# Optimization experiments

Hardware: AMD Instinct MI355X
Metric: run time of the kernel (lower is better)

Reference implementation:

```python
import jax, jax.numpy as jnp
import numpy as np

# ---- static config (matches init_kwargs) ----
B, L, D, H, NC = 2, 4096, 256, 8, 3
TOP_N, R = 8, 32              # top_n, vicinity_radius
LS, LE = 1000, 3000           # label_start, label_end
NL = 2                        # n_cross_attn_layers
FF = 4 * D                    # ffn_expand * d_model
Q_MAX = 2 * TOP_N * (2 * R + 1)  # 1040
HD = D // H


def setup_inputs() -> dict:
    key = jax.random.key(0)
    ks = jax.random.split(key, 12)
    def rn(k, shape, s=0.05):
        return jax.random.normal(k, shape, jnp.float32) * s
    return {
        "encoder_output": jax.random.normal(ks[0], (B, L, D), jnp.float32),
        "coarse_logits": jax.random.normal(ks[1], (B, L, NC), jnp.float32),
        "ln_q_g": jnp.ones((NL, D), jnp.float32),
        "ln_q_b": jnp.zeros((NL, D), jnp.float32),
        "ln_kv_g": jnp.ones((NL, D), jnp.float32),
        "ln_kv_b": jnp.zeros((NL, D), jnp.float32),
        "Wq": rn(ks[2], (NL, D, D)), "bq": jnp.zeros((NL, D), jnp.float32),
        "Wk": rn(ks[3], (NL, D, D)), "bk": jnp.zeros((NL, D), jnp.float32),
        "Wv": rn(ks[4], (NL, D, D)), "bv": jnp.zeros((NL, D), jnp.float32),
        "Wo": rn(ks[5], (NL, D, D)), "bo": jnp.zeros((NL, D), jnp.float32),
        "ffn_g": jnp.ones((NL, D), jnp.float32),
        "ffn_b": jnp.zeros((NL, D), jnp.float32),
        "W1": rn(ks[6], (NL, D, FF)), "b1": jnp.zeros((NL, FF), jnp.float32),
        "W2": rn(ks[7], (NL, FF, D)), "b2": jnp.zeros((NL, D), jnp.float32),
        "head_W": rn(ks[8], (D, NC)), "head_b": jnp.zeros((NC,), jnp.float32),
    }


def _layer_norm(x, g, b, eps=1e-5):
    m = jnp.mean(x, axis=-1, keepdims=True)
    v = jnp.mean(jnp.square(x - m), axis=-1, keepdims=True)
    return (x - m) * jax.lax.rsqrt(v + eps) * g + b


def _select_vicinities(coarse_logits):
    # eval mode: no gumbel noise. Returns (vicinity_idx (B,Q_MAX) int32 with
    # sentinel L at pad/dup slots, q_pad_mask (B,Q_MAX) bool).
    lp = jax.nn.log_softmax(coarse_logits.astype(jnp.float32), axis=-1)
    pos = jnp.arange(L)
    region = (pos >= LS) & (pos < LE)
    acc = jnp.where(region, lp[..., 1], -jnp.inf)
    don = jnp.where(region, lp[..., 2], -jnp.inf)
    _, don_idx = jax.lax.top_k(don, TOP_N)
    _, acc_idx = jax.lax.top_k(acc, TOP_N)
    centers = jnp.concatenate([don_idx, acc_idx], axis=-1)        # (B, 2*TOP_N)
    offsets = jnp.arange(-R, R + 1)
    vic = jnp.clip(centers[:, :, None] + offsets, 0, L - 1).reshape(B, -1)
    s = jnp.sort(vic, axis=-1)
    is_first = jnp.concatenate(
        [jnp.ones((B, 1), bool), s[:, 1:] != s[:, :-1]], axis=-1)
    idx = jnp.where(is_first, s, L)  # sentinel L -> zero row of scratch
    return idx, is_first


def reference(encoder_output, coarse_logits, ln_q_g, ln_q_b, ln_kv_g, ln_kv_b,
              Wq, bq, Wk, bk, Wv, bv, Wo, bo, ffn_g, ffn_b, W1, b1, W2, b2,
              head_W, head_b):
    idx, mask = _select_vicinities(coarse_logits)      # torch.no_grad() region
    idx = jax.lax.stop_gradient(idx)
    mask = jax.lax.stop_gradient(mask)

    scratch = jnp.pad(encoder_output, ((0, 0), (0, 1), (0, 0)))   # (B, L+1, D)
    q_stream = jnp.take_along_axis(scratch, idx[:, :, None], axis=1)  # (B,Q,D)
    kv = encoder_output
    m3 = mask[:, :, None]

    for i in range(NL):
        q_in = _layer_norm(q_stream, ln_q_g[i], ln_q_b[i])
        kv_in = _layer_norm(kv, ln_kv_g[i], ln_kv_b[i])
        q = (q_in @ Wq[i] + bq[i]).reshape(B, Q_MAX, H, HD)
        k = (kv_in @ Wk[i] + bk[i]).reshape(B, L, H, HD)
        v = (kv_in @ Wv[i] + bv[i]).reshape(B, L, H, HD)
        scores = jnp.einsum('bqhd,bkhd->bhqk', q, k) / jnp.sqrt(
            jnp.float32(HD))
        attn = jax.nn.softmax(scores, axis=-1)
        ao = jnp.einsum('bhqk,bkhd->bqhd', attn, v).reshape(B, Q_MAX, D)
        q_stream = q_stream + ao @ Wo[i] + bo[i]
        q_stream = jnp.where(m3, q_stream, 0.0)
        h = _layer_norm(q_stream, ffn_g[i], ffn_b[i])
        h = jax.nn.gelu(h @ W1[i] + b1[i], approximate=False) @ W2[i] + b2[i]
        q_stream = jnp.where(m3, q_stream + h, 0.0)

    out_scratch = scratch.at[jnp.arange(B)[:, None], idx].set(q_stream)
    refined = out_scratch[:, :L]                                  # drop sentinel
    refined_logits = refined @ head_W + head_b                    # (B, L, 3)
    return refined_logits
```

## Files before the change

kernel.cpp:

```cpp
#include <hip/hip_runtime.h>
#include <cmath>

constexpr int B = 2, L = 4096, D = 256, H = 8, NC = 3;
constexpr int TOP_N = 8, R = 32;
constexpr int LS = 1000, LE = 3000;
constexpr int NL = 2;
constexpr int FF = 4 * D;
constexpr int Q_MAX = 2 * TOP_N * (2 * R + 1);
constexpr int HD = D / H;
constexpr int QROWS = B * Q_MAX;
constexpr int KVROWS = B * L;
constexpr int NQT = (Q_MAX + 31) / 32;
constexpr int NREG = LE - LS;
constexpr int NSPLIT = 8;
constexpr int KCHUNK = L / NSPLIT;
constexpr int NT = KCHUNK / 32;
constexpr int KVBLK = 8 * (KVROWS / 64);
constexpr int QBLK = 4 * ((QROWS + 63) / 64);
constexpr int TRBLK = NL * 192;

typedef __attribute__((ext_vector_type(8))) short bf16x8;
typedef __attribute__((ext_vector_type(4))) float f32x4;
typedef __attribute__((ext_vector_type(4))) int i32x4;
typedef unsigned short u16;

union fr {
  bf16x8 h;
  i32x4 i;
};

__device__ __forceinline__ u16 f2bs(float f) {
  unsigned int u = __float_as_uint(f);
  unsigned int r = u + 0x7fffu + ((u >> 16) & 1u);
  return (u16)(r >> 16);
}
__device__ __forceinline__ float bs2f(u16 s) {
  return __uint_as_float(((unsigned int)s) << 16);
}
__device__ __forceinline__ float gelu_exact(float x) {
  return 0.5f * x * (1.f + erff(x * 0.70710678118654752440f));
}
__device__ __forceinline__ unsigned cvt_pk(float lo, float hi) {
  unsigned r;
  asm("v_cvt_pk_bf16_f32 %0, %1, %2" : "=v"(r) : "v"(lo), "v"(hi));
  return r;
}

#define GLL16(gsrc, ldst)                                                   \
  __builtin_amdgcn_global_load_lds(                                         \
      (const __attribute__((address_space(1))) unsigned int*)(gsrc),        \
      (__attribute__((address_space(3))) unsigned int*)(ldst), 16, 0, 0)

__global__ __launch_bounds__(256) void setup_kernel(
    const float* __restrict__ enc, const float* __restrict__ logits,
    const float* __restrict__ lnkvg, const float* __restrict__ lnkvb,
    const float* __restrict__ Wq_, const float* __restrict__ Wk_,
    const float* __restrict__ Wv_, const float* __restrict__ Wo_,
    const float* __restrict__ W1_, const float* __restrict__ W2_,
    u16* __restrict__ WT, u16* __restrict__ o0, u16* __restrict__ o1,
    int* __restrict__ idx_out, int* __restrict__ mask_out,
    int* __restrict__ inv_out) {
  int bid = blockIdx.x;
  int tid = threadIdx.x;
  const long DD = (long)D * D, DFF = (long)D * FF;
  const long LSTR = 4 * DD + 2 * DFF;

  if (bid < KVROWS) {
    long row = bid;
    float x = enc[row * D + tid];
    float s1 = x, s2 = x * x;
#pragma unroll
    for (int off = 32; off; off >>= 1) {
      s1 += __shfl_xor(s1, off, 64);
      s2 += __shfl_xor(s2, off, 64);
    }
    __shared__ float p1[4], p2[4];
    int w = tid >> 6;
    if ((tid & 63) == 0) { p1[w] = s1; p2[w] = s2; }
    __syncthreads();
    s1 = p1[0] + p1[1] + p1[2] + p1[3];
    s2 = p2[0] + p2[1] + p2[2] + p2[3];
    float mean = s1 * (1.f / D);
    float var = fmaxf(s2 * (1.f / D) - mean * mean, 0.f);
    float r = rsqrtf(var + 1e-5f);
    float xn = (x - mean) * r;
    o0[row * D + tid] = f2bs(xn * lnkvg[tid] + lnkvb[tid]);
    o1[row * D + tid] = f2bs(xn * lnkvg[D + tid] + lnkvb[D + tid]);
    return;
  }

  if (bid < KVROWS + TRBLK) {
    __shared__ u16 T[64][65];
    int t = bid - KVROWS;
    int l = t / 192, r = t % 192;
    const float* src;
    long dbase;
    int K_, N_, kt, nt;
    if (r < 64) {
      int which = r >> 4, sub = r & 15;
      kt = sub >> 2;
      nt = sub & 3;
      K_ = 256;
      N_ = 256;
      src = (which == 0 ? Wk_ : which == 1 ? Wv_ : which == 2 ? Wq_ : Wo_) +
            (long)l * DD;
      dbase = (long)l * LSTR + (long)which * DD;
    } else if (r < 128) {
      int sub = r - 64;
      kt = sub >> 4;
      nt = sub & 15;
      K_ = 256;
      N_ = 1024;
      src = W1_ + (long)l * DFF;
      dbase = (long)l * LSTR + 4 * DD;
    } else {
      int sub = r - 128;
      kt = sub >> 2;
      nt = sub & 3;
      K_ = 1024;
      N_ = 256;
      src = W2_ + (long)l * DFF;
      dbase = (long)l * LSTR + 4 * DD + DFF;
    }
    int k0 = kt * 64, n0 = nt * 64;
    {
      int kr = tid >> 2, c16 = (tid & 3) * 16;
      const float* sp = src + (long)(k0 + kr) * N_ + n0 + c16;
#pragma unroll
      for (int i = 0; i < 4; ++i) {
        float4 v = *reinterpret_cast<const float4*>(sp + 4 * i);
        T[kr][c16 + 4 * i + 0] = f2bs(v.x);
        T[kr][c16 + 4 * i + 1] = f2bs(v.y);
        T[kr][c16 + 4 * i + 2] = f2bs(v.z);
        T[kr][c16 + 4 * i + 3] = f2bs(v.w);
      }
    }
    __syncthreads();
    {
      int nr = tid >> 2, kc = (tid & 3) * 16;
      u16 tmp[16];
#pragma unroll
      for (int j = 0; j < 16; ++j) tmp[j] = T[kc + j][nr];
      u16* dp = WT + dbase + (long)(n0 + nr) * K_ + k0 + kc;
      *reinterpret_cast<bf16x8*>(dp) = *reinterpret_cast<const bf16x8*>(&tmp[0]);
      *reinterpret_cast<bf16x8*>(dp + 8) =
          *reinterpret_cast<const bf16x8*>(&tmp[8]);
    }
    return;
  }

  {
    int b = bid - KVROWS - TRBLK;
    int w = tid >> 6, lane = tid & 63;
    __shared__ float candv[4][8];
    __shared__ int candi[4][8];
    __shared__ int centers[2 * TOP_N];
    __shared__ unsigned present[L / 32];
    __shared__ int offs[128];
    __shared__ int wtot[2];

    float vd[8], va[8];
#pragma unroll
    for (int j = 0; j < 8; ++j) {
      int p = tid + j * 256;
      if (p < NREG) {
        const float* lg = logits + ((long)b * L + LS + p) * NC;
        float x0 = lg[0], x1 = lg[1], x2 = lg[2];
        float m = fmaxf(x0, fmaxf(x1, x2));
        float lse = m + logf(expf(x0 - m) + expf(x1 - m) + expf(x2 - m));
        vd[j] = x2 - lse;
        va[j] = x1 - lse;
      } else {
        vd[j] = -INFINITY;
        va[j] = -INFINITY;
      }
    }
    if (tid < 128) present[tid] = 0;
    for (int j = tid; j < L; j += 256) inv_out[(long)b * L + j] = -1;

    for (int sel = 0; sel < 2; ++sel) {
      float v[8];
#pragma unroll
      for (int j = 0; j < 8; ++j) v[j] = (sel == 0) ? vd[j] : va[j];
#pragma unroll
      for (int r = 0; r < TOP_N; ++r) {
        float mv = v[0];
        int mp = tid;
#pragma unroll
        for (int j = 1; j < 8; ++j) {
          int pj = tid + j * 256;
          if (v[j] > mv) { mv = v[j]; mp = pj; }
        }
#pragma unroll
        for (int off = 32; off; off >>= 1) {
          float ov = __shfl_xor(mv, off, 64);
          int oi = __shfl_xor(mp, off, 64);
          if (ov > mv || (ov == mv && oi < mp)) { mv = ov; mp = oi; }
        }
#pragma unroll
        for (int j = 0; j < 8; ++j)
          if (tid + j * 256 == mp) v[j] = -INFINITY;
        if (lane == 0) { candv[w][r] = mv; candi[w][r] = mp; }
      }
      __syncthreads();
      if (tid < 64) {
        float c = (tid < 32) ? candv[tid >> 3][tid & 7] : -INFINITY;
        int ci = (tid < 32) ? candi[tid >> 3][tid & 7] : 0x7fffffff;
#pragma unroll
        for (int r = 0; r < TOP_N; ++r) {
          float mv = c;
          int mi = ci;
#pragma unroll
          for (int off = 32; off; off >>= 1) {
            float ov = __shfl_xor(mv, off, 64);
            int oi = __shfl_xor(mi, off, 64);
            if (ov > mv || (ov == mv && oi < mi)) { mv = ov; mi = oi; }
          }
          if (ci == mi) c = -INFINITY;
          if (tid == 0) centers[sel * TOP_N + r] = LS + mi;
        }
      }
      __syncthreads();
    }

    for (int j = tid; j < Q_MAX; j += 256) {
      int c = centers[j / (2 * R + 1)];
      int off = j % (2 * R + 1) - R;
      int v2 = c + off;
      v2 = v2 < 0 ? 0 : (v2 > L - 1 ? L - 1 : v2);
      atomicOr(&present[v2 >> 5], 1u << (v2 & 31));
    }
    __syncthreads();

    int cnt = (tid < 128) ? __popc(present[tid]) : 0;
    if (tid < 128) {
      int x = cnt;
#pragma unroll
      for (int off = 1; off < 64; off <<= 1) {
        int o = __shfl_up(x, off, 64);
        if ((tid & 63) >= off) x += o;
      }
      if ((tid & 63) == 63) wtot[tid >> 6] = x;
      offs[tid] = x - cnt;
    }
    __syncthreads();
    int total = wtot[0] + wtot[1];
    if (tid < 128) {
      int base = offs[tid] + ((tid >= 64) ? wtot[0] : 0);
      unsigned mword = present[tid];
      while (mword) {
        int i = __ffs(mword) - 1;
        mword &= mword - 1;
        int pos = tid * 32 + i;
        idx_out[b * Q_MAX + base] = pos;
        mask_out[b * Q_MAX + base] = 1;
        inv_out[(long)b * L + pos] = b * Q_MAX + base;
        ++base;
      }
    }
    for (int j = total + tid; j < Q_MAX; j += 256) {
      idx_out[b * Q_MAX + j] = L;
      mask_out[b * Q_MAX + j] = 0;
    }
  }
}

__global__ __launch_bounds__(256) void gather_ln(
    const float* __restrict__ enc, const int* __restrict__ idx,
    float* __restrict__ q_stream, u16* __restrict__ q_ln,
    const float* __restrict__ gg, const float* __restrict__ bb) {
  int row = blockIdx.x;
  int b = row / Q_MAX;
  int p = idx[row];
  int tid = threadIdx.x;
  float x = 0.f;
  if (p < L) x = enc[((long)b * L + p) * D + tid];
  q_stream[(long)row * D + tid] = x;
  float s1 = x, s2 = x * x;
#pragma unroll
  for (int off = 32; off; off >>= 1) {
    s1 += __shfl_xor(s1, off, 64);
    s2 += __shfl_xor(s2, off, 64);
  }
  __shared__ float p1[4], p2[4];
  int w = tid >> 6;
  if ((tid & 63) == 0) { p1[w] = s1; p2[w] = s2; }
  __syncthreads();
  s1 = p1[0] + p1[1] + p1[2] + p1[3];
  s2 = p2[0] + p2[1] + p2[2] + p2[3];
  float mean = s1 * (1.f / D);
  float var = fmaxf(s2 * (1.f / D) - mean * mean, 0.f);
  float r = rsqrtf(var + 1e-5f);
  q_ln[(long)row * D + tid] = f2bs((x - mean) * r * gg[tid] + bb[tid]);
}

__global__ __launch_bounds__(256) void ln_bf16(
    const float* __restrict__ in, u16* __restrict__ out,
    const float* __restrict__ gg, const float* __restrict__ bb) {
  long row = blockIdx.x;
  int tid = threadIdx.x;
  float x = in[row * D + tid];
  float s1 = x, s2 = x * x;
#pragma unroll
  for (int off = 32; off; off >>= 1) {
    s1 += __shfl_xor(s1, off, 64);
    s2 += __shfl_xor(s2, off, 64);
  }
  __shared__ float p1[4], p2[4];
  int w = tid >> 6;
  if ((tid & 63) == 0) { p1[w] = s1; p2[w] = s2; }
  __syncthreads();
  s1 = p1[0] + p1[1] + p1[2] + p1[3];
  s2 = p2[0] + p2[1] + p2[2] + p2[3];
  float mean = s1 * (1.f / D);
  float var = fmaxf(s2 * (1.f / D) - mean * mean, 0.f);
  float r = rsqrtf(var + 1e-5f);
  out[row * D + tid] = f2bs((x - mean) * r * gg[tid] + bb[tid]);
}

template <int EPI>
__global__ __launch_bounds__(256) void gemm_mfma(
    const u16* __restrict__ A, const u16* __restrict__ BT,
    const float* __restrict__ bias, void* __restrict__ Cv,
    const float* __restrict__ resid, const int* __restrict__ mask, int M,
    int N, int K) {
  __shared__ short As[64][40];
  __shared__ short Bs[64][40];
  int bm = blockIdx.y * 64, bn = blockIdx.x * 64;
  int tid = threadIdx.x;
  int lane = tid & 63, w = tid >> 6;
  int g = lane >> 4, li = lane & 15;
  int wr = w >> 1, wc = w & 1;
  f32x4 acc[2][2] = {};

  int srow = tid >> 2, skc = (tid & 3) * 8;
  for (int k0 = 0; k0 < K; k0 += 32) {
    {
      int grow = bm + srow;
      bf16x8 av = {};
      if (grow < M)
        av = *reinterpret_cast<const bf16x8*>(A + (long)grow * K + k0 + skc);
      *reinterpret_cast<bf16x8*>(&As[srow][skc]) = av;
      bf16x8 bv = *reinterpret_cast<const bf16x8*>(
          BT + (long)(bn + srow) * K + k0 + skc);
      *reinterpret_cast<bf16x8*>(&Bs[srow][skc]) = bv;
    }
    __syncthreads();
    bf16x8 a0 = *reinterpret_cast<const bf16x8*>(&As[wr * 32 + li][g * 8]);
    bf16x8 a1 = *reinterpret_cast<const bf16x8*>(&As[wr * 32 + 16 + li][g * 8]);
    bf16x8 b0 = *reinterpret_cast<const bf16x8*>(&Bs[wc * 32 + li][g * 8]);
    bf16x8 b1 = *reinterpret_cast<const bf16x8*>(&Bs[wc * 32 + 16 + li][g * 8]);
    acc[0][0] = __builtin_amdgcn_mfma_f32_16x16x32_bf16(a0, b0, acc[0][0], 0, 0, 0);
    acc[0][1] = __builtin_amdgcn_mfma_f32_16x16x32_bf16(a0, b1, acc[0][1], 0, 0, 0);
    acc[1][0] = __builtin_amdgcn_mfma_f32_16x16x32_bf16(a1, b0, acc[1][0], 0, 0, 0);
    acc[1][1] = __builtin_amdgcn_mfma_f32_16x16x32_bf16(a1, b1, acc[1][1], 0, 0, 0);
    __syncthreads();
  }

#pragma unroll
  for (int mr = 0; mr < 2; ++mr)
#pragma unroll
    for (int nr = 0; nr < 2; ++nr)
#pragma unroll
      for (int r = 0; r < 4; ++r) {
        int row = bm + wr * 32 + mr * 16 + g * 4 + r;
        int col = bn + wc * 32 + nr * 16 + li;
        if (row >= M) continue;
        float v = acc[mr][nr][r] + bias[col];
        if (EPI == 1) v = gelu_exact(v);
        if (EPI == 2) {
          v += resid[(long)row * N + col];
          v = mask[row] ? v : 0.f;
          ((float*)Cv)[(long)row * N + col] = v;
        } else {
          ((u16*)Cv)[(long)row * N + col] = f2bs(v);
        }
      }
}

__global__ __launch_bounds__(256) void gemm_proj(
    const u16* __restrict__ Akv, const u16* __restrict__ Aq,
    const u16* __restrict__ WTbase, const float* __restrict__ biasK,
    const float* __restrict__ biasV, const float* __restrict__ biasQ,
    u16* __restrict__ Kh, u16* __restrict__ Vh, u16* __restrict__ Qb) {
  __shared__ short As[64][40];
  __shared__ short Bs[64][40];
  __shared__ u16 Ct[64][72];
  int bid = blockIdx.x;
  int tid = threadIdx.x;
  int lane = tid & 63, w = tid >> 6;
  int g = lane >> 4, li = lane & 15;
  int wr = w >> 1, wc = w & 1;
  f32x4 acc[2][2] = {};
  const long DD = (long)D * D;

  bool isKV = bid < KVBLK;
  int bm, bn, M;
  const u16* A;
  const u16* BT;
  if (isKV) {
    bn = (bid & 7) * 64;
    bm = (bid >> 3) * 64;
    M = KVROWS;
    A = Akv;
    BT = WTbase;
  } else {
    int qb = bid - KVBLK;
    bn = (qb & 3) * 64;
    bm = (qb >> 2) * 64;
    M = QROWS;
    A = Aq;
    BT = WTbase + 2 * DD;
  }

  int srow = tid >> 2, skc = (tid & 3) * 8;
  for (int k0 = 0; k0 < D; k0 += 32) {
    {
      int grow = bm + srow;
      bf16x8 av = {};
      if (grow < M)
        av = *reinterpret_cast<const bf16x8*>(A + (long)grow * D + k0 + skc);
      *reinterpret_cast<bf16x8*>(&As[srow][skc]) = av;
      bf16x8 bv = *reinterpret_cast<const bf16x8*>(
          BT + (long)(bn + srow) * D + k0 + skc);
      *reinterpret_cast<bf16x8*>(&Bs[srow][skc]) = bv;
    }
    __syncthreads();
    bf16x8 a0 = *reinterpret_cast<const bf16x8*>(&As[wr * 32 + li][g * 8]);
    bf16x8 a1 = *reinterpret_cast<const bf16x8*>(&As[wr * 32 + 16 + li][g * 8]);
    bf16x8 b0 = *reinterpret_cast<const bf16x8*>(&Bs[wc * 32 + li][g * 8]);
    bf16x8 b1 = *reinterpret_cast<const bf16x8*>(&Bs[wc * 32 + 16 + li][g * 8]);
    acc[0][0] = __builtin_amdgcn_mfma_f32_16x16x32_bf16(a0, b0, acc[0][0], 0, 0, 0);
    acc[0][1] = __builtin_amdgcn_mfma_f32_16x16x32_bf16(a0, b1, acc[0][1], 0, 0, 0);
    acc[1][0] = __builtin_amdgcn_mfma_f32_16x16x32_bf16(a1, b0, acc[1][0], 0, 0, 0);
    acc[1][1] = __builtin_amdgcn_mfma_f32_16x16x32_bf16(a1, b1, acc[1][1], 0, 0, 0);
    __syncthreads();
  }

  if (!isKV) {
#pragma unroll
    for (int mr = 0; mr < 2; ++mr)
#pragma unroll
      for (int nr = 0; nr < 2; ++nr)
#pragma unroll
        for (int r = 0; r < 4; ++r) {
          int row = bm + wr * 32 + mr * 16 + g * 4 + r;
          int col = bn + wc * 32 + nr * 16 + li;
          if (row >= M) continue;
          Qb[(long)row * D + col] = f2bs(acc[mr][nr][r] + biasQ[col]);
        }
  } else if (bn < 256) {
#pragma unroll
    for (int mr = 0; mr < 2; ++mr)
#pragma unroll
      for (int nr = 0; nr < 2; ++nr)
#pragma unroll
        for (int r = 0; r < 4; ++r) {
          int rowL = wr * 32 + mr * 16 + g * 4 + r;
          int colL = wc * 32 + nr * 16 + li;
          Ct[rowL][colL] = f2bs(acc[mr][nr][r] + biasK[bn + colL]);
        }
    __syncthreads();
#pragma unroll
    for (int p = 0; p < 2; ++p) {
      int rowL = (tid >> 3) + p * 32;
      int c8 = (tid & 7) * 8;
      int grow = bm + rowL;
      int b2 = grow >> 12, key = grow & (L - 1);
      int gcol = bn + c8;
      int hh = gcol >> 5, dd = gcol & (HD - 1);
      int cst = (dd >> 3) ^ ((key >> 1) & 3);
      u16* dst = Kh + (((long)(b2 * H + hh) * L + key) * 32 + (cst << 3));
      *reinterpret_cast<bf16x8*>(dst) =
          *reinterpret_cast<const bf16x8*>(&Ct[rowL][c8]);
    }
  } else {
    int vbn = bn - 256;
#pragma unroll
    for (int mr = 0; mr < 2; ++mr)
#pragma unroll
      for (int nr = 0; nr < 2; ++nr)
#pragma unroll
        for (int r = 0; r < 4; ++r) {
          int rowL = wr * 32 + mr * 16 + g * 4 + r;
          int colL = wc * 32 + nr * 16 + li;
          Ct[colL][rowL] = f2bs(acc[mr][nr][r] + biasV[vbn + colL]);
        }
    __syncthreads();
    int b2 = bm >> 12;
#pragma unroll
    for (int p = 0; p < 2; ++p) {
      int colL = (tid >> 3) + p * 32;
      int rem = tid & 7;
      int kb = rem >> 2, k8 = (rem & 3) * 8;
      int gcol = vbn + colL;
      int hh = gcol >> 5, dd = gcol & (HD - 1);
      int kb32 = ((bm & (L - 1)) >> 5) + kb;
      int j = (k8 >> 2) ^ ((dd >> 1) & 6);
      u16* dst = Vh + (((long)(b2 * H + hh) * (L / 32) + kb32) * 1024 +
                       dd * 32 + (j << 2));
      *reinterpret_cast<bf16x8*>(dst) =
          *reinterpret_cast<const bf16x8*>(&Ct[colL][kb * 32 + k8]);
    }
  }
}

constexpr int POOLSZ = NSPLIT * 32 * 33 * 4 + NSPLIT * 32 * 4;

__global__ __launch_bounds__(512) void attn_mfma(
    const u16* __restrict__ Qb, const u16* __restrict__ Kh,
    const u16* __restrict__ Vh, u16* __restrict__ AO) {
  __shared__ alignas(16) char pool[POOLSZ];
  int i = blockIdx.x;
  int xcd = i & 7, slot = i >> 3;
  int bh = (xcd << 1) | (slot >= NQT ? 1 : 0);
  int qt = (slot >= NQT) ? slot - NQT : slot;
  int h = bh & 7;
  int b = bh >> 3;
  int tid = threadIdx.x, w = tid >> 6, lane = tid & 63;
  int g = lane >> 4, li = lane & 15;

  fr qf0, qf1;
  {
    const float QSC = 0.25509836048f;
#pragma unroll
    for (int qb = 0; qb < 2; ++qb) {
      int qrow = qt * 32 + qb * 16 + li;
      if (qrow >= Q_MAX) qrow = Q_MAX - 1;
      bf16x8 raw = *reinterpret_cast<const bf16x8*>(
          Qb + ((long)(b * Q_MAX + qrow)) * D + h * HD + g * 8);
      fr& qf = qb ? qf1 : qf0;
#pragma unroll
      for (int j = 0; j < 4; ++j)
        qf.i[j] = (int)cvt_pk(bs2f((u16)raw[2 * j]) * QSC,
                              bs2f((u16)raw[2 * j + 1]) * QSC);
    }
  }

  f32x4 acc00 = {}, acc01 = {}, acc10 = {}, acc11 = {};
  float den0 = 0.f, den1 = 0.f;
  const f32x4 z = {};

  const u16* kbase = Kh + ((long)(b * H + h) * L) * HD;
  const u16* vbase = Vh + ((long)(b * H + h) * L) * HD;
  int kstart = w * KCHUNK;
  char* wbase = pool + w * 4096;

  int s_li = (li >> 1) & 3;
  int t_li = (li >> 1) & 6;
  int kof0 = li * 32 + ((g ^ s_li) << 3);
  int kof1 = (16 + li) * 32 + ((g ^ s_li) << 3);
  int va0o = li * 32 + ((g ^ t_li) << 2);
  int vb0o = li * 32 + (((4 + g) ^ t_li) << 2);
  int va1o = (16 + li) * 32 + ((g ^ t_li) << 2);
  int vb1o = (16 + li) * 32 + (((4 + g) ^ t_li) << 2);

  for (int t = 0; t < NT; ++t) {
    {
      const u16* ks = kbase + (long)(kstart + t * 32) * HD + lane * 8;
      const u16* vs = vbase + (long)(kstart + t * 32) * HD + lane * 8;
      u16* lk = (u16*)wbase;
      asm volatile("s_waitcnt lgkmcnt(0)" ::: "memory");
      GLL16(ks, lk);
      GLL16(ks + 512, lk + 512);
      GLL16(vs, lk + 1024);
      GLL16(vs + 512, lk + 1536);
      asm volatile("s_waitcnt vmcnt(0)" ::: "memory");
      __builtin_amdgcn_sched_barrier(0);
    }

    const u16* kl = (const u16*)wbase;
    const u16* vl = kl + 1024;
    bf16x8 kf0 = *reinterpret_cast<const bf16x8*>(kl + kof0);
    bf16x8 kf1 = *reinterpret_cast<const bf16x8*>(kl + kof1);
    uint2 va0 = *reinterpret_cast<const uint2*>(vl + va0o);
    uint2 vb0 = *reinterpret_cast<const uint2*>(vl + vb0o);
    uint2 va1 = *reinterpret_cast<const uint2*>(vl + va1o);
    uint2 vb1 = *reinterpret_cast<const uint2*>(vl + vb1o);

    f32x4 s00 = __builtin_amdgcn_mfma_f32_16x16x32_bf16(kf0, qf0.h, z, 0, 0, 0);
    f32x4 s10 = __builtin_amdgcn_mfma_f32_16x16x32_bf16(kf1, qf0.h, z, 0, 0, 0);
    f32x4 s01 = __builtin_amdgcn_mfma_f32_16x16x32_bf16(kf0, qf1.h, z, 0, 0, 0);
    f32x4 s11 = __builtin_amdgcn_mfma_f32_16x16x32_bf16(kf1, qf1.h, z, 0, 0, 0);

    float p00[4], p10[4], p01[4], p11[4];
#pragma unroll
    for (int r = 0; r < 4; ++r) {
      p00[r] = exp2f(s00[r]);
      p10[r] = exp2f(s10[r]);
      p01[r] = exp2f(s01[r]);
      p11[r] = exp2f(s11[r]);
      den0 += p00[r] + p10[r];
      den1 += p01[r] + p11[r];
    }
    fr pf0, pf1;
    pf0.i[0] = (int)cvt_pk(p00[0], p00[1]);
    pf0.i[1] = (int)cvt_pk(p00[2], p00[3]);
    pf0.i[2] = (int)cvt_pk(p10[0], p10[1]);
    pf0.i[3] = (int)cvt_pk(p10[2], p10[3]);
    pf1.i[0] = (int)cvt_pk(p01[0], p01[1]);
    pf1.i[1] = (int)cvt_pk(p01[2], p01[3]);
    pf1.i[2] = (int)cvt_pk(p11[0], p11[1]);
    pf1.i[3] = (int)cvt_pk(p11[2], p11[3]);

    fr v0, v1;
    v0.i = (i32x4){(int)va0.x, (int)va0.y, (int)vb0.x, (int)vb0.y};
    v1.i = (i32x4){(int)va1.x, (int)va1.y, (int)vb1.x, (int)vb1.y};
    acc00 = __builtin_amdgcn_mfma_f32_16x16x32_bf16(v0.h, pf0.h, acc00, 0, 0, 0);
    acc01 = __builtin_amdgcn_mfma_f32_16x16x32_bf16(v0.h, pf1.h, acc01, 0, 0, 0);
    acc10 = __builtin_amdgcn_mfma_f32_16x16x32_bf16(v1.h, pf0.h, acc10, 0, 0, 0);
    acc11 = __builtin_amdgcn_mfma_f32_16x16x32_bf16(v1.h, pf1.h, acc11, 0, 0, 0);
  }

  den0 += __shfl_xor(den0, 16, 64);
  den0 += __shfl_xor(den0, 32, 64);
  den1 += __shfl_xor(den1, 16, 64);
  den1 += __shfl_xor(den1, 32, 64);

  __syncthreads();
  float(*accs)[32][33] = (float(*)[32][33])pool;
  float(*dsh)[32] = (float(*)[32])(pool + NSPLIT * 32 * 33 * 4);
#pragma unroll
  for (int r = 0; r < 4; ++r) {
    accs[w][g * 4 + r][li] = acc00[r];
    accs[w][g * 4 + r][16 + li] = acc01[r];
    accs[w][16 + g * 4 + r][li] = acc10[r];
    accs[w][16 + g * 4 + r][16 + li] = acc11[r];
  }
  if (g == 0) {
    dsh[w][li] = den0;
    dsh[w][16 + li] = den1;
  }
  __syncthreads();

  int q = tid >> 4, dp = tid & 15;
  float Den = 0.f, o0 = 0.f, o1 = 0.f;
#pragma unroll
  for (int ww = 0; ww < NSPLIT; ++ww) {
    Den += dsh[ww][q];
    o0 += accs[ww][2 * dp][q];
    o1 += accs[ww][2 * dp + 1][q];
  }
  float inv = 1.f / Den;
  int qrow = qt * 32 + q;
  if (qrow < Q_MAX) {
    unsigned pk = cvt_pk(o0 * inv, o1 * inv);
    *reinterpret_cast<unsigned*>(
        AO + ((long)(b * Q_MAX + qrow)) * D + h * HD + 2 * dp) = pk;
  }
}

__global__ __launch_bounds__(256) void head_kernel(
    const float* __restrict__ enc, const float* __restrict__ q_stream,
    const int* __restrict__ inv, const float* __restrict__ hW,
    const float* __restrict__ hb, float* __restrict__ out) {
  int row = blockIdx.x * 4 + (threadIdx.x >> 6);
  int lane = threadIdx.x & 63;
  int slot = inv[row];
  const float* src =
      (slot >= 0) ? (q_stream + (long)slot * D) : (enc + (long)row * D);
  const float4 a = *reinterpret_cast<const float4*>(src + lane * 4);
  float c0 = 0.f, c1 = 0.f, c2 = 0.f;
  const float av[4] = {a.x, a.y, a.z, a.w};
#pragma unroll
  for (int i = 0; i < 4; ++i) {
    int k = lane * 4 + i;
    c0 += av[i] * hW[k * 3];
    c1 += av[i] * hW[k * 3 + 1];
    c2 += av[i] * hW[k * 3 + 2];
  }
#pragma unroll
  for (int off = 32; off; off >>= 1) {
    c0 += __shfl_down(c0, off, 64);
    c1 += __shfl_down(c1, off, 64);
    c2 += __shfl_down(c2, off, 64);
  }
  if (lane == 0) {
    out[(long)row * 3] = c0 + hb[0];
    out[(long)row * 3 + 1] = c1 + hb[1];
    out[(long)row * 3 + 2] = c2 + hb[2];
  }
}

extern "C" void kernel_launch(void* const* d_in, const int* in_sizes, int n_in,
                              void* d_out, int out_size, void* d_ws,
                              size_t ws_size, hipStream_t stream) {
  const float* enc = (const float*)d_in[0];
  const float* clog = (const float*)d_in[1];
  const float* ln_q_g = (const float*)d_in[2];
  const float* ln_q_b = (const float*)d_in[3];
  const float* ln_kv_g = (const float*)d_in[4];
  const float* ln_kv_b = (const float*)d_in[5];
  const float* Wq = (const float*)d_in[6];
  const float* bq = (const float*)d_in[7];
  const float* Wk = (const float*)d_in[8];
  const float* bk = (const float*)d_in[9];
  const float* Wv = (const float*)d_in[10];
  const float* bv = (const float*)d_in[11];
  const float* Wo = (const float*)d_in[12];
  const float* bo = (const float*)d_in[13];
  const float* ffn_g = (const float*)d_in[14];
  const float* ffn_b = (const float*)d_in[15];
  const float* W1 = (const float*)d_in[16];
  const float* b1 = (const float*)d_in[17];
  const float* W2 = (const float*)d_in[18];
  const float* b2 = (const float*)d_in[19];
  const float* head_W = (const float*)d_in[20];
  const float* head_b = (const float*)d_in[21];
  float* out = (float*)d_out;

  char* ws = (char*)d_ws;
  float* q_stream = (float*)ws;            ws += (long)QROWS * D * 4;
  u16* kvl0 = (u16*)ws;                    ws += (long)KVROWS * D * 2;
  u16* kvl1 = (u16*)ws;                    ws += (long)KVROWS * D * 2;
  u16* Khbuf = (u16*)ws;                   ws += (long)B * H * L * HD * 2;
  u16* Vhbuf = (u16*)ws;                   ws += (long)B * H * L * HD * 2;
  u16* q_ln = (u16*)ws;                    ws += (long)QROWS * D * 2;
  u16* Qbuf = (u16*)ws;                    ws += (long)QROWS * D * 2;
  u16* AObuf = (u16*)ws;                   ws += (long)QROWS * D * 2;
  u16* H1buf = (u16*)ws;                   ws += (long)QROWS * FF * 2;
  u16* WT = (u16*)ws;                      ws += (long)NL * (4 * D * D + 2 * D * FF) * 2;
  int* idxbuf = (int*)ws;                  ws += QROWS * 4;
  int* maskbuf = (int*)ws;                 ws += QROWS * 4;
  int* invbuf = (int*)ws;                  ws += (long)B * L * 4;

  const long DD = (long)D * D, DFF = (long)D * FF;
  const long LSTR = 4 * DD + 2 * DFF;

  setup_kernel<<<KVROWS + TRBLK + B, 256, 0, stream>>>(
      enc, clog, ln_kv_g, ln_kv_b, Wq, Wk, Wv, Wo, W1, W2, WT, kvl0, kvl1,
      idxbuf, maskbuf, invbuf);
  gather_ln<<<QROWS, 256, 0, stream>>>(enc, idxbuf, q_stream, q_ln, ln_q_g,
                                       ln_q_b);

  for (int l = 0; l < NL; ++l) {
    u16* base = WT + l * LSTR;
    u16* kv_ln = (l == 0) ? kvl0 : kvl1;

    if (l > 0)
      ln_bf16<<<QROWS, 256, 0, stream>>>(q_stream, q_ln, ln_q_g + l * D,
                                         ln_q_b + l * D);

    gemm_proj<<<KVBLK + QBLK, 256, 0, stream>>>(
        kv_ln, q_ln, base, bk + l * D, bv + l * D, bq + l * D, Khbuf, Vhbuf,
        Qbuf);

    attn_mfma<<<B * H * NQT, 512, 0, stream>>>(Qbuf, Khbuf, Vhbuf, AObuf);

    dim3 gQ(D / 64, (QROWS + 63) / 64);
    gemm_mfma<2><<<gQ, 256, 0, stream>>>(AObuf, base + 3 * DD, bo + l * D,
                                         (void*)q_stream, q_stream, maskbuf,
                                         QROWS, D, D);

    ln_bf16<<<QROWS, 256, 0, stream>>>(q_stream, q_ln, ffn_g + l * D, ffn_b + l * D);
    dim3 gF1(FF / 64, (QROWS + 63) / 64);
    gemm_mfma<1><<<gF1, 256, 0, stream>>>(q_ln, base + 4 * DD, b1 + l * FF,
                                          (void*)H1buf, nullptr, nullptr,
                                          QROWS, FF, D);
    dim3 gF2(D / 64, (QROWS + 63) / 64);
    gemm_mfma<2><<<gF2, 256, 0, stream>>>(H1buf, base + 4 * DD + DFF,
                                          b2 + l * D, (void*)q_stream,
                                          q_stream, maskbuf, QROWS, D, FF);
  }

  head_kernel<<<KVROWS / 4, 256, 0, stream>>>(enc, q_stream, invbuf, head_W,
                                              head_b, out);
}
```

Baseline: 222.2 us.

## Software-pipeline K/V tile loads in attention loop with staggered waits

The attention inner loop now issues the global-to-LDS load for the next K tile right after the current K fragments are read into registers, and does the same for the next V tile after V is read. Before this, each iteration waited for all loads to finish before any compute. Split vmcnt waits let the next tile's loads overlap the current tile's MFMA and exp work. The cost is more delicate waitcnt ordering over a single LDS buffer per wave.

Result: no change. 219.3 us (-1.3%).

```diff
diff --git a/kernel.cpp b/kernel.cpp
--- a/kernel.cpp
+++ b/kernel.cpp
@@ -555,33 +555,41 @@
   int va1o = (16 + li) * 32 + ((g ^ t_li) << 2);
   int vb1o = (16 + li) * 32 + (((4 + g) ^ t_li) << 2);
 
+  {
+    const u16* ks = kbase + (long)kstart * HD + lane * 8;
+    const u16* vs = vbase + (long)kstart * HD + lane * 8;
+    u16* lk = (u16*)wbase;
+    GLL16(ks, lk);
+    GLL16(ks + 512, lk + 512);
+    GLL16(vs, lk + 1024);
+    GLL16(vs + 512, lk + 1536);
+  }
+
   for (int t = 0; t < NT; ++t) {
-    {
-      const u16* ks = kbase + (long)(kstart + t * 32) * HD + lane * 8;
-      const u16* vs = vbase + (long)(kstart + t * 32) * HD + lane * 8;
+    const u16* kl = (const u16*)wbase;
+    const u16* vl = kl + 1024;
+
+    asm volatile("s_waitcnt vmcnt(2)" ::: "memory");
+    __builtin_amdgcn_sched_barrier(0);
+    fr kf0, kf1;
+    kf0.h = *reinterpret_cast<const bf16x8*>(kl + kof0);
+    kf1.h = *reinterpret_cast<const bf16x8*>(kl + kof1);
+    asm volatile("" ::"v"(kf0.i[0]), "v"(kf0.i[1]), "v"(kf0.i[2]),
+                 "v"(kf0.i[3]), "v"(kf1.i[0]), "v"(kf1.i[1]), "v"(kf1.i[2]),
+                 "v"(kf1.i[3]));
+    asm volatile("s_waitcnt lgkmcnt(0)" ::: "memory");
+    __builtin_amdgcn_sched_barrier(0);
+    if (t + 1 < NT) {
+      const u16* ks = kbase + (long)(kstart + (t + 1) * 32) * HD + lane * 8;
       u16* lk = (u16*)wbase;
-      asm volatile("s_waitcnt lgkmcnt(0)" ::: "memory");
       GLL16(ks, lk);
       GLL16(ks + 512, lk + 512);
-      GLL16(vs, lk + 1024);
-      GLL16(vs + 512, lk + 1536);
-      asm volatile("s_waitcnt vmcnt(0)" ::: "memory");
-      __builtin_amdgcn_sched_barrier(0);
-    }
-
-    const u16* kl = (const u16*)wbase;
-    const u16* vl = kl + 1024;
-    bf16x8 kf0 = *reinterpret_cast<const bf16x8*>(kl + kof0);
-    bf16x8 kf1 = *reinterpret_cast<const bf16x8*>(kl + kof1);
-    uint2 va0 = *reinterpret_cast<const uint2*>(vl + va0o);
-    uint2 vb0 = *reinterpret_cast<const uint2*>(vl + vb0o);
-    uint2 va1 = *reinterpret_cast<const uint2*>(vl + va1o);
-    uint2 vb1 = *reinterpret_cast<const uint2*>(vl + vb1o);
-
-    f32x4 s00 = __builtin_amdgcn_mfma_f32_16x16x32_bf16(kf0, qf0.h, z, 0, 0, 0);
-    f32x4 s10 = __builtin_amdgcn_mfma_f32_16x16x32_bf16(kf1, qf0.h, z, 0, 0, 0);
-    f32x4 s01 = __builtin_amdgcn_mfma_f32_16x16x32_bf16(kf0, qf1.h, z, 0, 0, 0);
-    f32x4 s11 = __builtin_amdgcn_mfma_f32_16x16x32_bf16(kf1, qf1.h, z, 0, 0, 0);
+    }
+
+    f32x4 s00 = __builtin_amdgcn_mfma_f32_16x16x32_bf16(kf0.h, qf0.h, z, 0, 0, 0);
+    f32x4 s10 = __builtin_amdgcn_mfma_f32_16x16x32_bf16(kf1.h, qf0.h, z, 0, 0, 0);
+    f32x4 s01 = __builtin_amdgcn_mfma_f32_16x16x32_bf16(kf0.h, qf1.h, z, 0, 0, 0);
+    f32x4 s11 = __builtin_amdgcn_mfma_f32_16x16x32_bf16(kf1.h, qf1.h, z, 0, 0, 0);
 
     float p00[4], p10[4], p01[4], p11[4];
 #pragma unroll
@@ -602,6 +610,26 @@
     pf1.i[1] = (int)cvt_pk(p01[2], p01[3]);
     pf1.i[2] = (int)cvt_pk(p11[0], p11[1]);
     pf1.i[3] = (int)cvt_pk(p11[2], p11[3]);
+
+    if (t + 1 < NT)
+      asm volatile("s_waitcnt vmcnt(2)" ::: "memory");
+    else
+      asm volatile("s_waitcnt vmcnt(0)" ::: "memory");
+    __builtin_amdgcn_sched_barrier(0);
+    uint2 va0 = *reinterpret_cast<const uint2*>(vl + va0o);
+    uint2 vb0 = *reinterpret_cast<const uint2*>(vl + vb0o);
+    uint2 va1 = *reinterpret_cast<const uint2*>(vl + va1o);
+    uint2 vb1 = *reinterpret_cast<const uint2*>(vl + vb1o);
+    asm volatile("" ::"v"(va0.x), "v"(va0.y), "v"(vb0.x), "v"(vb0.y),
+                 "v"(va1.x), "v"(va1.y), "v"(vb1.x), "v"(vb1.y));
+    asm volatile("s_waitcnt lgkmcnt(0)" ::: "memory");
+    __builtin_amdgcn_sched_barrier(0);
+    if (t + 1 < NT) {
+      const u16* vs = vbase + (long)(kstart + (t + 1) * 32) * HD + lane * 8;
+      u16* lk = (u16*)wbase;
+      GLL16(vs, lk + 1024);
+      GLL16(vs + 512, lk + 1536);
+    }
 
     fr v0, v1;
     v0.i = (i32x4){(int)va0.x, (int)va0.y, (int)vb0.x, (int)vb0.y};
```
